# Optimization experiments

Measured on AMD Instinct MI355X. Metric: run time of the kernel, lower is better.

Reference implementation:

```python
import jax, jax.numpy as jnp
import numpy as np

ALPHA = 1.702
LIMIT = 7.0


def setup_inputs() -> dict:
    E, H, D = 16, 2880, 2880
    B, S = 2, 1024
    T = B * S
    key = jax.random.key(0)
    ks = jax.random.split(key, 8)
    hidden_states = jax.random.normal(ks[0], (B, S, H), dtype=jnp.float32)
    routing_weights = jax.random.uniform(ks[1], (T, E), dtype=jnp.float32)
    scale = 0.02
    Wg = jax.random.normal(ks[2], (E, H, D), dtype=jnp.float32) * scale
    bg = jax.random.normal(ks[3], (E, D), dtype=jnp.float32) * scale
    Wu = jax.random.normal(ks[4], (E, H, D), dtype=jnp.float32) * scale
    bu = jax.random.normal(ks[5], (E, D), dtype=jnp.float32) * scale
    Wd = jax.random.normal(ks[6], (E, D, H), dtype=jnp.float32) * scale
    bd = jax.random.normal(ks[7], (E, H), dtype=jnp.float32) * scale
    return {"hidden_states": hidden_states, "routing_weights": routing_weights,
            "Wg": Wg, "bg": bg, "Wu": Wu, "bu": bu, "Wd": Wd, "bd": bd}


def reference(hidden_states, routing_weights, Wg, bg, Wu, bu, Wd, bd):
    orig_shape = hidden_states.shape
    H = Wg.shape[1]
    x = hidden_states.reshape(-1, H)  # [T, H]
    # per-expert gate/up projections: [E, T, D]
    gate = jnp.einsum('th,ehd->etd', x, Wg) + bg[:, None, :]
    gate = jnp.minimum(gate, LIMIT)
    up = jnp.einsum('th,ehd->etd', x, Wu) + bu[:, None, :]
    up = jnp.clip(up, -LIMIT, LIMIT)
    glu = gate * jax.nn.sigmoid(gate * ALPHA)
    inter = (up + 1.0) * glu  # [E, T, D]
    # down projection: [E, T, H]
    down = jnp.einsum('etd,edh->eth', inter, Wd) + bd[:, None, :]
    # routing-weighted sum over experts: [T, H]
    out = jnp.einsum('eth,te->th', down, routing_weights)
    return out.reshape(orig_shape)
```

## Files before the change

kernel.cpp:

```cpp
#include <hip/hip_runtime.h>
#include <cstdint>


#define ALPHA 1.702f
#define LIMIT 7.0f

static constexpr int E = 16;
static constexpr int H = 2880;
static constexpr int D = 2880;
static constexpr int T = 2048;
static constexpr int NKT = 45;
static constexpr int DP  = 3072;
static constexpr int NPR = 2*DP;

typedef float        f32x4  __attribute__((ext_vector_type(4)));
typedef short        bf16x8 __attribute__((ext_vector_type(8)));

#define MFMA_BF16(a,b,c) __builtin_amdgcn_mfma_f32_16x16x32_bf16((a),(b),(c),0,0,0)
#define SBAR()        __builtin_amdgcn_s_barrier()
#define SCHED_FENCE() __builtin_amdgcn_sched_barrier(0)
#define PRIO1()       __builtin_amdgcn_s_setprio(1)
#define PRIO0()       __builtin_amdgcn_s_setprio(0)
#define LGK0()        asm volatile("s_waitcnt lgkmcnt(0)" ::: "memory")
#define VMC6()        asm volatile("s_waitcnt vmcnt(6)" ::: "memory")

__device__ __forceinline__ unsigned short f2bf(float f){
  unsigned u = __builtin_bit_cast(unsigned, f);
  u += 0x7fffu + ((u >> 16) & 1u);
  return (unsigned short)(u >> 16);
}
__device__ __forceinline__ unsigned pack2(float a, float b){
  return (unsigned)f2bf(a) | ((unsigned)f2bf(b) << 16);
}

__device__ __forceinline__ void gload_lds16(const void* g, void* l){
  __builtin_amdgcn_global_load_lds((const __attribute__((address_space(1))) unsigned*)g,
                                   (__attribute__((address_space(3))) unsigned*)l,
                                   16, 0, 0);
}

__global__ void cvt_kernel(const float* __restrict__ in, unsigned short* __restrict__ ob, int n8){
  int i = blockIdx.x * 256 + threadIdx.x;
  if (i < n8){
    float4 a = ((const float4*)in)[2*i];
    float4 b = ((const float4*)in)[2*i+1];
    uint4 o;
    o.x = pack2(a.x, a.y); o.y = pack2(a.z, a.w);
    o.z = pack2(b.x, b.y); o.w = pack2(b.z, b.w);
    ((uint4*)ob)[i] = o;
  }
}

__global__ __launch_bounds__(256) void tcvt_kernel(
    const float* __restrict__ src, unsigned short* __restrict__ dst,
    int mode, size_t dstStride)
{
  __shared__ unsigned short tl[64*72];
  const int t = threadIdx.x;
  const float* s = src + (size_t)blockIdx.z * H * D;
  unsigned short* o = dst + (size_t)blockIdx.z * dstStride;
  const int r0 = blockIdx.x * 64, c0 = blockIdx.y * 64;

  if (c0 < D){
    int rr = t >> 2;
    #pragma unroll
    for (int p = 0; p < 4; ++p){
      int cc = ((t & 3) + p*4) * 4;
      float4 v = *(const float4*)(s + (size_t)(r0 + rr)*D + c0 + cc);
      tl[(cc+0)*72 + rr] = f2bf(v.x);
      tl[(cc+1)*72 + rr] = f2bf(v.y);
      tl[(cc+2)*72 + rr] = f2bf(v.z);
      tl[(cc+3)*72 + rr] = f2bf(v.w);
    }
    __syncthreads();
    #pragma unroll
    for (int p = 0; p < 2; ++p){
      int task = p*256 + t;
      int cl = task >> 3, ch = task & 7;
      int c = c0 + cl;
      int rowp = (mode < 2) ? ((c >> 5)*64 + (c & 31) + mode*32) : c;
      bf16x8 v = *(const bf16x8*)&tl[cl*72 + ch*8];
      *(bf16x8*)(o + (size_t)rowp*H + r0 + ch*8) = v;
    }
  } else {
    #pragma unroll
    for (int p = 0; p < 2; ++p){
      int task = p*256 + t;
      int cl = task >> 3, ch = task & 7;
      int c = c0 + cl;
      int rowp = (mode < 2) ? ((c >> 5)*64 + (c & 31) + mode*32) : c;
      bf16x8 z = (bf16x8){0,0,0,0,0,0,0,0};
      *(bf16x8*)(o + (size_t)rowp*H + r0 + ch*8) = z;
    }
  }
}

__global__ void reduce_kernel(const float* __restrict__ p, float* __restrict__ out,
                              int n4, int nz){
  int i = blockIdx.x * 256 + threadIdx.x;
  if (i < n4){
    f32x4 a = ((const f32x4*)p)[i];
    for (int g = 1; g < nz; ++g)
      a += ((const f32x4*)(p + (size_t)g * T * H))[i];
    ((f32x4*)out)[i] = a;
  }
}

__global__ __launch_bounds__(512, 2) void gateup_kernel(
    const unsigned short* __restrict__ xb,
    const unsigned short* __restrict__ wGU,
    const float* __restrict__ bg,
    const float* __restrict__ bu,
    const float* __restrict__ rw,
    unsigned short* __restrict__ inter,
    int e0)
{
  __shared__ short As[2][256*64];
  __shared__ short Bs[2][256*64];

  const int t = threadIdx.x, lane = t & 63, wv = t >> 6;
  const int wm = wv >> 2, wn = wv & 3;

  int nbx = gridDim.x, nby = gridDim.y;
  int lin = blockIdx.x + nbx*(blockIdx.y + nby*blockIdx.z);
  int per = (nbx*nby*gridDim.z) >> 3;
  int id2 = (lin & 7)*per + (lin >> 3);
  int bx = id2 % nbx; int rem = id2 / nbx;
  int by = rem % nby; int ez = rem / nby;

  const int trow0 = bx*256, ncol0 = by*256;
  const int e = e0 + ez;
  const unsigned short* wg = wGU + (size_t)ez * NPR * H;

  f32x4 acc[8][4];
  #pragma unroll
  for (int i = 0; i < 8; ++i)
    #pragma unroll
    for (int j = 0; j < 4; ++j) acc[i][j] = (f32x4){0.f,0.f,0.f,0.f};

  auto stageA = [&](int kt, int b, int h){
    #pragma unroll
    for (int r2 = 0; r2 < 2; ++r2){
      int task = r2*512 + t;
      int ps = task >> 3, ch = task & 7, sch = ch ^ (ps & 7);
      int lr = h*64 + (ps & 63) + ((ps >> 6) << 7);
      gload_lds16(xb + (size_t)(trow0 + lr)*H + kt*64 + sch*8,
                  &As[b][h*8192 + task*8]);
    }
  };
  auto stageB = [&](int kt, int b, int h){
    #pragma unroll
    for (int r2 = 0; r2 < 2; ++r2){
      int task = r2*512 + t;
      int ps = task >> 3, ch = task & 7, sch = ch ^ (ps & 7);
      int lr = h*32 + ((ps >> 5) << 6) + (ps & 31);
      gload_lds16(wg + (size_t)(ncol0 + lr)*H + kt*64 + sch*8,
                  &Bs[b][h*8192 + task*8]);
    }
  };

  bf16x8 af[4][2], bLo[2][2], bHi[2][2];
  auto readAh = [&](int b, int qa){
    #pragma unroll
    for (int mi = 0; mi < 4; ++mi){
      int r = wm*128 + qa*64 + mi*16 + (lane & 15);
      int q = r >> 6, qs = ((q & 1) << 1) | (q >> 1);
      int pr = qs*64 + (r & 63);
      #pragma unroll
      for (int kk = 0; kk < 2; ++kk){
        int pc = (kk*4 + (lane >> 4)) ^ (pr & 7);
        af[mi][kk] = *(const bf16x8*)&As[b][pr*64 + pc*8];
      }
    }
  };
  auto readBh = [&](bf16x8 (&bf)[2][2], int b, int hb){
    #pragma unroll
    for (int ni = 0; ni < 2; ++ni){
      int rB = wn*64 + hb*32 + ni*16 + (lane & 15);
      int pr = ((rB >> 5) & 1)*128 + (rB >> 6)*32 + (rB & 31);
      #pragma unroll
      for (int kk = 0; kk < 2; ++kk){
        int pc = (kk*4 + (lane >> 4)) ^ (pr & 7);
        bf[ni][kk] = *(const bf16x8*)&Bs[b][pr*64 + pc*8];
      }
    }
  };
  auto mfmaQ = [&](bf16x8 (&bf)[2][2], int qa, int hb){
    #pragma unroll
    for (int kk = 0; kk < 2; ++kk)
      #pragma unroll
      for (int ni = 0; ni < 2; ++ni)
        #pragma unroll
        for (int mi = 0; mi < 4; ++mi)
          acc[qa*4+mi][hb*2+ni] = MFMA_BF16(af[mi][kk], bf[ni][kk], acc[qa*4+mi][hb*2+ni]);
  };

  stageA(0,0,0); stageB(0,0,0); stageB(0,0,1); stageA(0,0,1);
  stageA(1,1,0); stageB(1,1,0); stageB(1,1,1);
  asm volatile("s_waitcnt vmcnt(8)" ::: "memory");
  SBAR();

  for (int it = 0; it < 22; ++it){
    int kt = 2*it;
    int ktA = (kt+2 < NKT) ? kt+2 : NKT-1;
    int ktB = (kt+3 < NKT) ? kt+3 : NKT-1;
    readAh(0, 0); readBh(bLo, 0, 0);
    stageA(kt+1, 1, 1);
    SCHED_FENCE(); SBAR(); LGK0(); SCHED_FENCE();
    PRIO1(); mfmaQ(bLo, 0, 0); PRIO0();
    VMC6(); SBAR();
    readBh(bHi, 0, 1);
    stageA(ktA, 0, 0);
    SCHED_FENCE(); SBAR(); LGK0(); SCHED_FENCE();
    PRIO1(); mfmaQ(bHi, 0, 1); PRIO0();
    VMC6(); SBAR();
    readAh(0, 1);
    stageB(ktA, 0, 0);
    SCHED_FENCE(); SBAR(); LGK0(); SCHED_FENCE();
    PRIO1(); mfmaQ(bHi, 1, 1); PRIO0();
    VMC6(); SBAR();
    stageB(ktA, 0, 1);
    SCHED_FENCE(); SBAR(); SCHED_FENCE();
    PRIO1(); mfmaQ(bLo, 1, 0); PRIO0();
    VMC6(); SBAR();
    readAh(1, 0); readBh(bLo, 1, 0);
    stageA(ktA, 0, 1);
    SCHED_FENCE(); SBAR(); LGK0(); SCHED_FENCE();
    PRIO1(); mfmaQ(bLo, 0, 0); PRIO0();
    VMC6(); SBAR();
    readBh(bHi, 1, 1);
    stageA(ktB, 1, 0);
    SCHED_FENCE(); SBAR(); LGK0(); SCHED_FENCE();
    PRIO1(); mfmaQ(bHi, 0, 1); PRIO0();
    VMC6(); SBAR();
    readAh(1, 1);
    stageB(ktB, 1, 0);
    SCHED_FENCE(); SBAR(); LGK0(); SCHED_FENCE();
    PRIO1(); mfmaQ(bHi, 1, 1); PRIO0();
    VMC6(); SBAR();
    stageB(ktB, 1, 1);
    SCHED_FENCE(); SBAR(); SCHED_FENCE();
    PRIO1(); mfmaQ(bLo, 1, 0); PRIO0();
    VMC6(); SBAR();
  }

  asm volatile("s_waitcnt vmcnt(0)" ::: "memory");
  SBAR();
  readAh(0, 0); readBh(bLo, 0, 0); readBh(bHi, 0, 1);
  LGK0(); SCHED_FENCE();
  mfmaQ(bLo, 0, 0); mfmaQ(bHi, 0, 1);
  readAh(0, 1);
  LGK0(); SCHED_FENCE();
  mfmaQ(bHi, 1, 1); mfmaQ(bLo, 1, 0);

  const float* bgp = bg + (size_t)e * D;
  const float* bup = bu + (size_t)e * D;
  unsigned short* ip = inter + (size_t)ez * T * D;
  const int dbase = (by*4 + wn) * 32;
  #pragma unroll
  for (int g = 0; g < 2; ++g){
    int d0 = dbase + g*16;
    if (d0 < D){
      int d = d0 + (lane & 15);
      float bgv = bgp[d], buv = bup[d];
      #pragma unroll
      for (int mi = 0; mi < 8; ++mi){
        #pragma unroll
        for (int r = 0; r < 4; ++r){
          int trw = trow0 + wm*128 + mi*16 + (lane >> 4)*4 + r;
          float gv = acc[mi][g][r] + bgv;
          float uv = acc[mi][g+2][r] + buv;
          gv = fminf(gv, LIMIT);
          uv = fminf(fmaxf(uv, -LIMIT), LIMIT);
          float glu = gv / (1.f + __expf(-ALPHA * gv));
          float rv = rw[trw*E + e];
          ip[(size_t)trw * D + d] = f2bf(rv * (uv + 1.f) * glu);
        }
      }
    }
  }
}

__global__ __launch_bounds__(512, 2) void down_kernel(
    const unsigned short* __restrict__ inter,
    const unsigned short* __restrict__ wdT,
    const float* __restrict__ bd,
    const float* __restrict__ rw,
    float* __restrict__ pout,
    int e0)
{
  __shared__ short As[2][256*64];
  __shared__ short Bs[2][256*64];

  const int t = threadIdx.x, lane = t & 63, wv = t >> 6;
  const int wm = wv >> 2, wn = wv & 3;

  int nbx = gridDim.x, nby = gridDim.y;
  int lin = blockIdx.x + nbx*(blockIdx.y + nby*blockIdx.z);
  int per = (nbx*nby*gridDim.z) >> 3;
  int id2 = (lin & 7)*per + (lin >> 3);
  int bx = id2 % nbx; int rem = id2 / nbx;
  int by = rem % nby; int ez = rem / nby;

  const int trow0 = bx*256, ncol0 = by*256;
  const int e = e0 + ez;
  const unsigned short* ap = inter + (size_t)ez * T * D;
  const unsigned short* wd = wdT + (size_t)ez * DP * D;

  f32x4 acc[8][4];
  #pragma unroll
  for (int i = 0; i < 8; ++i)
    #pragma unroll
    for (int j = 0; j < 4; ++j) acc[i][j] = (f32x4){0.f,0.f,0.f,0.f};

  auto stageA = [&](int kt, int b, int h){
    #pragma unroll
    for (int r2 = 0; r2 < 2; ++r2){
      int task = r2*512 + t;
      int ps = task >> 3, ch = task & 7, sch = ch ^ (ps & 7);
      int lr = h*64 + (ps & 63) + ((ps >> 6) << 7);
      gload_lds16(ap + (size_t)(trow0 + lr)*D + kt*64 + sch*8,
                  &As[b][h*8192 + task*8]);
    }
  };
  auto stageB = [&](int kt, int b, int h){
    #pragma unroll
    for (int r2 = 0; r2 < 2; ++r2){
      int task = r2*512 + t;
      int ps = task >> 3, ch = task & 7, sch = ch ^ (ps & 7);
      int lr = h*32 + ((ps >> 5) << 6) + (ps & 31);
      gload_lds16(wd + (size_t)(ncol0 + lr)*D + kt*64 + sch*8,
                  &Bs[b][h*8192 + task*8]);
    }
  };

  bf16x8 af[4][2], bLo[2][2], bHi[2][2];
  auto readAh = [&](int b, int qa){
    #pragma unroll
    for (int mi = 0; mi < 4; ++mi){
      int r = wm*128 + qa*64 + mi*16 + (lane & 15);
      int q = r >> 6, qs = ((q & 1) << 1) | (q >> 1);
      int pr = qs*64 + (r & 63);
      #pragma unroll
      for (int kk = 0; kk < 2; ++kk){
        int pc = (kk*4 + (lane >> 4)) ^ (pr & 7);
        af[mi][kk] = *(const bf16x8*)&As[b][pr*64 + pc*8];
      }
    }
  };
  auto readBh = [&](bf16x8 (&bf)[2][2], int b, int hb){
    #pragma unroll
    for (int ni = 0; ni < 2; ++ni){
      int rB = wn*64 + hb*32 + ni*16 + (lane & 15);
      int pr = ((rB >> 5) & 1)*128 + (rB >> 6)*32 + (rB & 31);
      #pragma unroll
      for (int kk = 0; kk < 2; ++kk){
        int pc = (kk*4 + (lane >> 4)) ^ (pr & 7);
        bf[ni][kk] = *(const bf16x8*)&Bs[b][pr*64 + pc*8];
      }
    }
  };
  auto mfmaQ = [&](bf16x8 (&bf)[2][2], int qa, int hb){
    #pragma unroll
    for (int kk = 0; kk < 2; ++kk)
      #pragma unroll
      for (int ni = 0; ni < 2; ++ni)
        #pragma unroll
        for (int mi = 0; mi < 4; ++mi)
          acc[qa*4+mi][hb*2+ni] = MFMA_BF16(af[mi][kk], bf[ni][kk], acc[qa*4+mi][hb*2+ni]);
  };

  stageA(0,0,0); stageB(0,0,0); stageB(0,0,1); stageA(0,0,1);
  stageA(1,1,0); stageB(1,1,0); stageB(1,1,1);
  asm volatile("s_waitcnt vmcnt(8)" ::: "memory");
  SBAR();

  for (int it = 0; it < 22; ++it){
    int kt = 2*it;
    int ktA = (kt+2 < NKT) ? kt+2 : NKT-1;
    int ktB = (kt+3 < NKT) ? kt+3 : NKT-1;
    readAh(0, 0); readBh(bLo, 0, 0);
    stageA(kt+1, 1, 1);
    SCHED_FENCE(); SBAR(); LGK0(); SCHED_FENCE();
    PRIO1(); mfmaQ(bLo, 0, 0); PRIO0();
    VMC6(); SBAR();
    readBh(bHi, 0, 1);
    stageA(ktA, 0, 0);
    SCHED_FENCE(); SBAR(); LGK0(); SCHED_FENCE();
    PRIO1(); mfmaQ(bHi, 0, 1); PRIO0();
    VMC6(); SBAR();
    readAh(0, 1);
    stageB(ktA, 0, 0);
    SCHED_FENCE(); SBAR(); LGK0(); SCHED_FENCE();
    PRIO1(); mfmaQ(bHi, 1, 1); PRIO0();
    VMC6(); SBAR();
    stageB(ktA, 0, 1);
    SCHED_FENCE(); SBAR(); SCHED_FENCE();
    PRIO1(); mfmaQ(bLo, 1, 0); PRIO0();
    VMC6(); SBAR();
    readAh(1, 0); readBh(bLo, 1, 0);
    stageA(ktA, 0, 1);
    SCHED_FENCE(); SBAR(); LGK0(); SCHED_FENCE();
    PRIO1(); mfmaQ(bLo, 0, 0); PRIO0();
    VMC6(); SBAR();
    readBh(bHi, 1, 1);
    stageA(ktB, 1, 0);
    SCHED_FENCE(); SBAR(); LGK0(); SCHED_FENCE();
    PRIO1(); mfmaQ(bHi, 0, 1); PRIO0();
    VMC6(); SBAR();
    readAh(1, 1);
    stageB(ktB, 1, 0);
    SCHED_FENCE(); SBAR(); LGK0(); SCHED_FENCE();
    PRIO1(); mfmaQ(bHi, 1, 1); PRIO0();
    VMC6(); SBAR();
    stageB(ktB, 1, 1);
    SCHED_FENCE(); SBAR(); SCHED_FENCE();
    PRIO1(); mfmaQ(bLo, 1, 0); PRIO0();
    VMC6(); SBAR();
  }

  asm volatile("s_waitcnt vmcnt(0)" ::: "memory");
  SBAR();
  readAh(0, 0); readBh(bLo, 0, 0); readBh(bHi, 0, 1);
  LGK0(); SCHED_FENCE();
  mfmaQ(bLo, 0, 0); mfmaQ(bHi, 0, 1);
  readAh(0, 1);
  LGK0(); SCHED_FENCE();
  mfmaQ(bHi, 1, 1); mfmaQ(bLo, 1, 0);

  const float* bdp = bd + (size_t)e * H;
  float* pp = pout + (size_t)ez * T * H;
  const int accum = (e0 != 0);
  #pragma unroll
  for (int j = 0; j < 4; ++j){
    int h0 = ncol0 + wn*64 + j*16;
    if (h0 < H){
      int h = h0 + (lane & 15);
      float bdv = bdp[h];
      #pragma unroll
      for (int mi = 0; mi < 8; ++mi){
        #pragma unroll
        for (int r = 0; r < 4; ++r){
          int trw = trow0 + wm*128 + mi*16 + (lane >> 4)*4 + r;
          float rv = rw[trw*E + e];
          size_t oi = (size_t)trw * H + h;
          float v = acc[mi][j][r] + rv * bdv;
          if (accum) v += pp[oi];
          pp[oi] = v;
        }
      }
    }
  }
}

extern "C" void kernel_launch(void* const* d_in, const int* in_sizes, int n_in,
                              void* d_out, int out_size, void* d_ws, size_t ws_size,
                              hipStream_t stream) {
  const float* hs  = (const float*)d_in[0];
  const float* rwt = (const float*)d_in[1];
  const float* Wg  = (const float*)d_in[2];
  const float* bg  = (const float*)d_in[3];
  const float* Wu  = (const float*)d_in[4];
  const float* bu  = (const float*)d_in[5];
  const float* Wd  = (const float*)d_in[6];
  const float* bd  = (const float*)d_in[7];
  float* out = (float*)d_out;

  const size_t xbytes = (size_t)T * H * 2;
  const size_t interB = (size_t)T * D * 2;
  const size_t guB    = (size_t)NPR * H * 2;
  const size_t wdB    = (size_t)DP * D * 2;
  const size_t poutE  = (size_t)T * H * 4;
  const size_t perE   = interB + guB + wdB + poutE;

  long long avail = (long long)ws_size - (long long)xbytes;
  int EC = (int)(avail / (long long)perE);
  if (EC < 1) EC = 1;
  if (EC > E) EC = E;

  unsigned short* xb    = (unsigned short*)d_ws;
  float*          pout  = (float*)((char*)d_ws + xbytes);
  unsigned short* inter = (unsigned short*)((char*)d_ws + xbytes + (size_t)EC*poutE);
  unsigned short* wGU   = inter + (size_t)EC * T * D;
  unsigned short* wdT   = wGU + (size_t)EC * NPR * H;

  cvt_kernel<<<(T*H/8 + 255)/256, 256, 0, stream>>>(hs, xb, T*H/8);

  for (int e0 = 0; e0 < E; e0 += EC){
    int ec = (E - e0 < EC) ? (E - e0) : EC;
    tcvt_kernel<<<dim3(45,48,ec), 256, 0, stream>>>(Wg + (size_t)e0*H*D, wGU, 0, (size_t)NPR*H);
    tcvt_kernel<<<dim3(45,48,ec), 256, 0, stream>>>(Wu + (size_t)e0*H*D, wGU, 1, (size_t)NPR*H);
    gateup_kernel<<<dim3(8, 24, ec), 512, 0, stream>>>(xb, wGU, bg, bu, rwt, inter, e0);
    tcvt_kernel<<<dim3(45,48,ec), 256, 0, stream>>>(Wd + (size_t)e0*H*D, wdT, 2, (size_t)DP*D);
    down_kernel<<<dim3(8, 12, ec), 512, 0, stream>>>(inter, wdT, bd, rwt, pout, e0);
  }
  reduce_kernel<<<(T*H/4 + 255)/256, 256, 0, stream>>>(pout, out, T*H/4, EC);
}
```

Before: 2.134 ms.

## Fuse experts into one long-K down GEMM with split-K partials

The down projection no longer runs one GEMM per expert. The gate/up kernel now writes each expert's intermediate into a concatenated K dimension (EC*D), and the down weights are laid out to match, so a single down GEMM covers all experts in a chunk and sums over them. That GEMM is split along K into four partial buffers, which cuts the fp32 partial output storage from EC to four slices. The routing-weighted down bias moves into the final reduce kernel, and the gate/up grid is trimmed so it skips padding columns. The trade-off is a longer K loop per block, split-K reduction traffic, and an expert chunk that must be a multiple of four.

```diff
diff --git a/kernel.cpp b/kernel.cpp
--- a/kernel.cpp
+++ b/kernel.cpp
@@ -10,8 +10,9 @@
 static constexpr int D = 2880;
 static constexpr int T = 2048;
 static constexpr int NKT = 45;
-static constexpr int DP  = 3072;
-static constexpr int NPR = 2*DP;
+static constexpr int NPR = 5888;
+static constexpr int HP  = 3072;
+static constexpr int NZ  = 4;
 
 typedef float        f32x4  __attribute__((ext_vector_type(4)));
 typedef short        bf16x8 __attribute__((ext_vector_type(8)));
@@ -53,12 +54,12 @@
 
 __global__ __launch_bounds__(256) void tcvt_kernel(
     const float* __restrict__ src, unsigned short* __restrict__ dst,
-    int mode, size_t dstStride)
+    int mode, size_t expStride, size_t rowStride)
 {
   __shared__ unsigned short tl[64*72];
   const int t = threadIdx.x;
   const float* s = src + (size_t)blockIdx.z * H * D;
-  unsigned short* o = dst + (size_t)blockIdx.z * dstStride;
+  unsigned short* o = dst + (size_t)blockIdx.z * expStride;
   const int r0 = blockIdx.x * 64, c0 = blockIdx.y * 64;
 
   if (c0 < D){
@@ -80,7 +81,7 @@
       int c = c0 + cl;
       int rowp = (mode < 2) ? ((c >> 5)*64 + (c & 31) + mode*32) : c;
       bf16x8 v = *(const bf16x8*)&tl[cl*72 + ch*8];
-      *(bf16x8*)(o + (size_t)rowp*H + r0 + ch*8) = v;
+      *(bf16x8*)(o + (size_t)rowp*rowStride + r0 + ch*8) = v;
     }
   } else {
     #pragma unroll
@@ -90,18 +91,29 @@
       int c = c0 + cl;
       int rowp = (mode < 2) ? ((c >> 5)*64 + (c & 31) + mode*32) : c;
       bf16x8 z = (bf16x8){0,0,0,0,0,0,0,0};
-      *(bf16x8*)(o + (size_t)rowp*H + r0 + ch*8) = z;
-    }
-  }
-}
-
-__global__ void reduce_kernel(const float* __restrict__ p, float* __restrict__ out,
-                              int n4, int nz){
+      *(bf16x8*)(o + (size_t)rowp*rowStride + r0 + ch*8) = z;
+    }
+  }
+}
+
+__global__ void reduce_kernel(const float* __restrict__ p,
+                              const float* __restrict__ rw,
+                              const float* __restrict__ bd,
+                              float* __restrict__ out, int n4){
   int i = blockIdx.x * 256 + threadIdx.x;
   if (i < n4){
+    int t  = i / (H/4);
+    int h4 = (i % (H/4)) * 4;
     f32x4 a = ((const f32x4*)p)[i];
-    for (int g = 1; g < nz; ++g)
-      a += ((const f32x4*)(p + (size_t)g * T * H))[i];
+    #pragma unroll
+    for (int z = 1; z < NZ; ++z)
+      a += ((const f32x4*)(p + (size_t)z * T * H))[i];
+    #pragma unroll
+    for (int e = 0; e < E; ++e){
+      float r = rw[t*E + e];
+      f32x4 b = *(const f32x4*)(bd + (size_t)e*H + h4);
+      a += r * b;
+    }
     ((f32x4*)out)[i] = a;
   }
 }
@@ -113,7 +125,7 @@
     const float* __restrict__ bu,
     const float* __restrict__ rw,
     unsigned short* __restrict__ inter,
-    int e0)
+    int e0, int KD)
 {
   __shared__ short As[2][256*64];
   __shared__ short Bs[2][256*64];
@@ -255,7 +267,7 @@
 
   const float* bgp = bg + (size_t)e * D;
   const float* bup = bu + (size_t)e * D;
-  unsigned short* ip = inter + (size_t)ez * T * D;
+  unsigned short* ip = inter + (size_t)ez * D;
   const int dbase = (by*4 + wn) * 32;
   #pragma unroll
   for (int g = 0; g < 2; ++g){
@@ -274,7 +286,7 @@
           uv = fminf(fmaxf(uv, -LIMIT), LIMIT);
           float glu = gv / (1.f + __expf(-ALPHA * gv));
           float rv = rw[trw*E + e];
-          ip[(size_t)trw * D + d] = f2bf(rv * (uv + 1.f) * glu);
+          ip[(size_t)trw * KD + d] = f2bf(rv * (uv + 1.f) * glu);
         }
       }
     }
@@ -283,11 +295,9 @@
 
 __global__ __launch_bounds__(512, 2) void down_kernel(
     const unsigned short* __restrict__ inter,
-    const unsigned short* __restrict__ wdT,
-    const float* __restrict__ bd,
-    const float* __restrict__ rw,
+    const unsigned short* __restrict__ wdA,
     float* __restrict__ pout,
-    int e0)
+    int nk64, int KD, int accum)
 {
   __shared__ short As[2][256*64];
   __shared__ short Bs[2][256*64];
@@ -300,12 +310,11 @@
   int per = (nbx*nby*gridDim.z) >> 3;
   int id2 = (lin & 7)*per + (lin >> 3);
   int bx = id2 % nbx; int rem = id2 / nbx;
-  int by = rem % nby; int ez = rem / nby;
+  int by = rem % nby; int z  = rem / nby;
 
   const int trow0 = bx*256, ncol0 = by*256;
-  const int e = e0 + ez;
-  const unsigned short* ap = inter + (size_t)ez * T * D;
-  const unsigned short* wd = wdT + (size_t)ez * DP * D;
+  const int ksteps = nk64 >> 2;
+  const int kst = z * ksteps, kend = kst + ksteps;
 
   f32x4 acc[8][4];
   #pragma unroll
@@ -319,7 +328,7 @@
       int task = r2*512 + t;
       int ps = task >> 3, ch = task & 7, sch = ch ^ (ps & 7);
       int lr = h*64 + (ps & 63) + ((ps >> 6) << 7);
-      gload_lds16(ap + (size_t)(trow0 + lr)*D + kt*64 + sch*8,
+      gload_lds16(inter + (size_t)(trow0 + lr)*KD + kt*64 + sch*8,
                   &As[b][h*8192 + task*8]);
     }
   };
@@ -329,7 +338,7 @@
       int task = r2*512 + t;
       int ps = task >> 3, ch = task & 7, sch = ch ^ (ps & 7);
       int lr = h*32 + ((ps >> 5) << 6) + (ps & 31);
-      gload_lds16(wd + (size_t)(ncol0 + lr)*D + kt*64 + sch*8,
+      gload_lds16(wdA + (size_t)(ncol0 + lr)*KD + kt*64 + sch*8,
                   &Bs[b][h*8192 + task*8]);
     }
   };
@@ -370,15 +379,16 @@
           acc[qa*4+mi][hb*2+ni] = MFMA_BF16(af[mi][kk], bf[ni][kk], acc[qa*4+mi][hb*2+ni]);
   };
 
-  stageA(0,0,0); stageB(0,0,0); stageB(0,0,1); stageA(0,0,1);
-  stageA(1,1,0); stageB(1,1,0); stageB(1,1,1);
+  stageA(kst,0,0); stageB(kst,0,0); stageB(kst,0,1); stageA(kst,0,1);
+  stageA(kst+1,1,0); stageB(kst+1,1,0); stageB(kst+1,1,1);
   asm volatile("s_waitcnt vmcnt(8)" ::: "memory");
   SBAR();
 
-  for (int it = 0; it < 22; ++it){
-    int kt = 2*it;
-    int ktA = (kt+2 < NKT) ? kt+2 : NKT-1;
-    int ktB = (kt+3 < NKT) ? kt+3 : NKT-1;
+  const int nit = (ksteps - 1) >> 1;
+  for (int it = 0; it < nit; ++it){
+    int kt = kst + 2*it;
+    int ktA = (kt+2 < kend) ? kt+2 : kend-1;
+    int ktB = (kt+3 < kend) ? kt+3 : kend-1;
     readAh(0, 0); readBh(bLo, 0, 0);
     stageA(kt+1, 1, 1);
     SCHED_FENCE(); SBAR(); LGK0(); SCHED_FENCE();
@@ -419,32 +429,34 @@
     VMC6(); SBAR();
   }
 
+  if ((ksteps & 1) == 0)
+    stageA(kend-1, 1, 1);
+
   asm volatile("s_waitcnt vmcnt(0)" ::: "memory");
   SBAR();
-  readAh(0, 0); readBh(bLo, 0, 0); readBh(bHi, 0, 1);
-  LGK0(); SCHED_FENCE();
-  mfmaQ(bLo, 0, 0); mfmaQ(bHi, 0, 1);
-  readAh(0, 1);
-  LGK0(); SCHED_FENCE();
-  mfmaQ(bHi, 1, 1); mfmaQ(bLo, 1, 0);
-
-  const float* bdp = bd + (size_t)e * H;
-  float* pp = pout + (size_t)ez * T * H;
-  const int accum = (e0 != 0);
+  for (int jt = 2*nit; jt < ksteps; ++jt){
+    int b = jt & 1;
+    readAh(b, 0); readBh(bLo, b, 0); readBh(bHi, b, 1);
+    LGK0(); SCHED_FENCE();
+    mfmaQ(bLo, 0, 0); mfmaQ(bHi, 0, 1);
+    readAh(b, 1);
+    LGK0(); SCHED_FENCE();
+    mfmaQ(bHi, 1, 1); mfmaQ(bLo, 1, 0);
+  }
+
+  float* pp = pout + (size_t)z * T * H;
   #pragma unroll
   for (int j = 0; j < 4; ++j){
     int h0 = ncol0 + wn*64 + j*16;
     if (h0 < H){
       int h = h0 + (lane & 15);
-      float bdv = bdp[h];
       #pragma unroll
       for (int mi = 0; mi < 8; ++mi){
         #pragma unroll
         for (int r = 0; r < 4; ++r){
           int trw = trow0 + wm*128 + mi*16 + (lane >> 4)*4 + r;
-          float rv = rw[trw*E + e];
           size_t oi = (size_t)trw * H + h;
-          float v = acc[mi][j][r] + rv * bdv;
+          float v = acc[mi][j][r];
           if (accum) v += pp[oi];
           pp[oi] = v;
         }
@@ -467,32 +479,36 @@
   float* out = (float*)d_out;
 
   const size_t xbytes = (size_t)T * H * 2;
-  const size_t interB = (size_t)T * D * 2;
-  const size_t guB    = (size_t)NPR * H * 2;
-  const size_t wdB    = (size_t)DP * D * 2;
-  const size_t poutE  = (size_t)T * H * 4;
-  const size_t perE   = interB + guB + wdB + poutE;
-
-  long long avail = (long long)ws_size - (long long)xbytes;
+  const size_t poutB  = (size_t)NZ * T * H * 4;
+  const size_t perE = (size_t)T*D*2 + (size_t)NPR*H*2 + (size_t)HP*D*2;
+
+  long long avail = (long long)ws_size - (long long)(xbytes + poutB);
   int EC = (int)(avail / (long long)perE);
-  if (EC < 1) EC = 1;
   if (EC > E) EC = E;
+  EC -= EC % 4;
+  if (EC < 4) EC = 4;
+  const int KD = EC * D;
 
   unsigned short* xb    = (unsigned short*)d_ws;
   float*          pout  = (float*)((char*)d_ws + xbytes);
-  unsigned short* inter = (unsigned short*)((char*)d_ws + xbytes + (size_t)EC*poutE);
-  unsigned short* wGU   = inter + (size_t)EC * T * D;
-  unsigned short* wdT   = wGU + (size_t)EC * NPR * H;
+  unsigned short* inter = (unsigned short*)((char*)d_ws + xbytes + poutB);
+  unsigned short* wGU   = inter + (size_t)T * KD;
+  unsigned short* wdA   = wGU + (size_t)EC * NPR * H;
 
   cvt_kernel<<<(T*H/8 + 255)/256, 256, 0, stream>>>(hs, xb, T*H/8);
 
   for (int e0 = 0; e0 < E; e0 += EC){
     int ec = (E - e0 < EC) ? (E - e0) : EC;
-    tcvt_kernel<<<dim3(45,48,ec), 256, 0, stream>>>(Wg + (size_t)e0*H*D, wGU, 0, (size_t)NPR*H);
-    tcvt_kernel<<<dim3(45,48,ec), 256, 0, stream>>>(Wu + (size_t)e0*H*D, wGU, 1, (size_t)NPR*H);
-    gateup_kernel<<<dim3(8, 24, ec), 512, 0, stream>>>(xb, wGU, bg, bu, rwt, inter, e0);
-    tcvt_kernel<<<dim3(45,48,ec), 256, 0, stream>>>(Wd + (size_t)e0*H*D, wdT, 2, (size_t)DP*D);
-    down_kernel<<<dim3(8, 12, ec), 512, 0, stream>>>(inter, wdT, bd, rwt, pout, e0);
-  }
-  reduce_kernel<<<(T*H/4 + 255)/256, 256, 0, stream>>>(pout, out, T*H/4, EC);
-}
+    tcvt_kernel<<<dim3(45,46,ec), 256, 0, stream>>>(
+        Wg + (size_t)e0*H*D, wGU, 0, (size_t)NPR*H, (size_t)H);
+    tcvt_kernel<<<dim3(45,46,ec), 256, 0, stream>>>(
+        Wu + (size_t)e0*H*D, wGU, 1, (size_t)NPR*H, (size_t)H);
+    tcvt_kernel<<<dim3(45,48,ec), 256, 0, stream>>>(
+        Wd + (size_t)e0*H*D, wdA, 2, (size_t)D, (size_t)KD);
+    gateup_kernel<<<dim3(8, 23, ec), 512, 0, stream>>>(
+        xb, wGU, bg, bu, rwt, inter, e0, KD);
+    down_kernel<<<dim3(8, 12, NZ), 512, 0, stream>>>(
+        inter, wdA, pout, ec*NKT, KD, e0 != 0);
+  }
+  reduce_kernel<<<(T*H/4 + 255)/256, 256, 0, stream>>>(pout, rwt, bd, out, T*H/4);
+}
```

Result: no change. 2.112 ms (-1.0%).
